# Kernel optimization log

Hardware: AMD Instinct MI355X
Metric: run time of the kernel (lower is better)

Reference implementation:

```python
import jax, jax.numpy as jnp
import numpy as np

BETA = 0.25  # commitment loss weight (standard VQ-VAE)


def setup_inputs() -> dict:
    key = jax.random.key(0)
    ks = jax.random.split(key, 6)
    B, C, H, W = 8, 64, 64, 64
    K = 8192  # codebook size
    return {
        "z": jax.random.normal(ks[0], (B, C, H, W), dtype=jnp.float32),
        "pre_w": jax.random.normal(ks[1], (C, C), dtype=jnp.float32) * (1.0 / np.sqrt(C)),
        "pre_b": jax.random.normal(ks[2], (C,), dtype=jnp.float32) * 0.02,
        "emb": jax.random.normal(ks[3], (K, C), dtype=jnp.float32),
        "post_w": jax.random.normal(ks[4], (C, C), dtype=jnp.float32) * (1.0 / np.sqrt(C)),
        "post_b": jax.random.normal(ks[5], (C,), dtype=jnp.float32) * 0.02,
    }


def reference(z, pre_w, pre_b, emb, post_w, post_b):
    B, C, H, W = z.shape
    # pre_quant_conv: 1x1 conv == channel-mixing matmul
    ze = jnp.einsum("bchw,oc->bohw", z, pre_w) + pre_b[None, :, None, None]
    # flatten to tokens [N, C]
    zf = ze.transpose(0, 2, 3, 1).reshape(-1, C)
    # squared L2 distances to codebook: ||z||^2 - 2 z.e + ||e||^2
    d = (jnp.sum(zf * zf, axis=1, keepdims=True)
         - 2.0 * (zf @ emb.T)
         + jnp.sum(emb * emb, axis=1)[None, :])  # [N, K]
    idx = jnp.argmin(d, axis=1)  # [N]
    q = emb[idx].reshape(B, H, W, C).transpose(0, 3, 1, 2)  # [B,C,H,W]
    # VQ losses
    codebook_loss = jnp.mean((jax.lax.stop_gradient(ze) - q) ** 2)
    commit_loss = BETA * jnp.mean((ze - jax.lax.stop_gradient(q)) ** 2)
    loss = codebook_loss + commit_loss
    # straight-through estimator
    quant = ze + jax.lax.stop_gradient(q - ze)
    # post_quant_conv: 1x1 conv
    out = jnp.einsum("bchw,oc->bohw", quant, post_w) + post_b[None, :, None, None]
    return out, loss
```

## Files before the change

### kernel.cpp

```cpp
#include <hip/hip_runtime.h>
#include <stdint.h>

#define HW 4096
#define NTOK 32768
#define KCB 8192
#define YSPLIT 8
#define KCOV (KCB / YSPLIT)
#define NCHUNK (KCOV / 64)
#define MARGIN 0.0119628906f

typedef __bf16 bf16x8 __attribute__((ext_vector_type(8)));
typedef float f32x16 __attribute__((ext_vector_type(16)));
typedef unsigned int uint;
typedef unsigned short u16;
typedef unsigned long long u64;

static __device__ inline u16 f2bf(float f) {
    uint u = __float_as_uint(f);
    return (u16)((u + 0x7FFFu + ((u >> 16) & 1u)) >> 16);
}
static __device__ inline float bf2f(u16 h) {
    return __uint_as_float(((uint)h) << 16);
}
static __device__ inline uint fsort(float f) {
    uint u = __float_as_uint(f);
    return u ^ ((uint)((int)u >> 31) | 0x80000000u);
}
static __device__ inline uint umin2(uint a, uint b) { return a < b ? a : b; }
static __device__ inline uint umax2(uint a, uint b) { return a > b ? a : b; }
static __device__ inline uint umed3(uint a, uint b, uint c) {
    return umax2(umin2(a, b), umin2(umax2(a, b), c));
}

__global__ __launch_bounds__(256) void prep_kernel(
    const float* __restrict__ z, const float* __restrict__ pre_w,
    const float* __restrict__ pre_b, const float* __restrict__ emb,
    u16* __restrict__ zq, u16* __restrict__ embq,
    float* __restrict__ ee, float* __restrict__ eebs,
    float* __restrict__ loss_out, int* __restrict__ flagcnt)
{
    __shared__ __attribute__((aligned(16))) float wt[64 * 64];
    __shared__ __attribute__((aligned(16))) float zt[64 * 64];
    __shared__ float bls[64];
    const int t  = threadIdx.x;
    const int bx = blockIdx.x;

    if (bx >= 512) {
        const int k   = (bx - 512) * 32 + (t >> 3);
        const int sub = t & 7;
        const float4* er = (const float4*)(emb + (size_t)k * 64 + sub * 8);
        float4 v0 = er[0], v1 = er[1];

        float s = v0.x*v0.x + v0.y*v0.y + v0.z*v0.z + v0.w*v0.w
                + v1.x*v1.x + v1.y*v1.y + v1.z*v1.z + v1.w*v1.w;
        s += __shfl_xor(s, 1, 64);
        s += __shfl_xor(s, 2, 64);
        s += __shfl_xor(s, 4, 64);
        if (sub == 0) { ee[k] = s; eebs[k] = 1024.f * (256.f + s); }

        float vals[8] = {-64.f*v0.x, -64.f*v0.y, -64.f*v0.z, -64.f*v0.w,
                         -64.f*v1.x, -64.f*v1.y, -64.f*v1.z, -64.f*v1.w};
        u16 hb[8], lb[8];
        #pragma unroll
        for (int c = 0; c < 8; ++c) {
            hb[c] = f2bf(vals[c]);
            lb[c] = f2bf(vals[c] - bf2f(hb[c]));
        }
        uint4 uh, ul;
        uh.x = (uint)hb[0] | ((uint)hb[1] << 16);
        uh.y = (uint)hb[2] | ((uint)hb[3] << 16);
        uh.z = (uint)hb[4] | ((uint)hb[5] << 16);
        uh.w = (uint)hb[6] | ((uint)hb[7] << 16);
        ul.x = (uint)lb[0] | ((uint)lb[1] << 16);
        ul.y = (uint)lb[2] | ((uint)lb[3] << 16);
        ul.z = (uint)lb[4] | ((uint)lb[5] << 16);
        ul.w = (uint)lb[6] | ((uint)lb[7] << 16);

        const int sw = k & 7;
        uint4* out = (uint4*)(embq + (size_t)k * 128);
        out[sub ^ sw]       = uh;
        out[(8 + sub) ^ sw] = ul;
        if (bx == 512 && t == 0) { loss_out[0] = 0.f; *flagcnt = 0; }
        return;
    }

    const int tok0 = bx * 64;
    const int b    = tok0 >> 12;
    const int hw0  = tok0 & 4095;

    for (int i = t; i < 64 * 64; i += 256) {
        int o = i >> 6, c = i & 63;
        wt[c * 64 + o] = pre_w[i];
    }
    if (t < 64) bls[t] = pre_b[t];
    {
        const int tl = t & 63;
        #pragma unroll
        for (int rr = 0; rr < 16; ++rr) {
            const int c = (t >> 6) + rr * 4;
            zt[c * 64 + tl] = z[(size_t)b * (64 * HW) + (size_t)c * HW + hw0 + tl];
        }
    }
    __syncthreads();

    const int tok = t >> 2;
    const int og  = t & 3;
    const int n   = tok0 + tok;

    float acc[16];
    #pragma unroll
    for (int j = 0; j < 16; ++j) acc[j] = 0.f;

    for (int c = 0; c < 64; ++c) {
        const float zv = zt[c * 64 + tok];
        #pragma unroll
        for (int g = 0; g < 4; ++g) {
            float4 w4 = *(const float4*)(wt + c * 64 + og * 16 + g * 4);
            acc[g*4+0] = fmaf(zv, w4.x, acc[g*4+0]);
            acc[g*4+1] = fmaf(zv, w4.y, acc[g*4+1]);
            acc[g*4+2] = fmaf(zv, w4.z, acc[g*4+2]);
            acc[g*4+3] = fmaf(zv, w4.w, acc[g*4+3]);
        }
    }
    #pragma unroll
    for (int j = 0; j < 16; ++j) acc[j] = 32.f * (acc[j] + bls[og * 16 + j]);

    uint uh[8], ul[8];
    #pragma unroll
    for (int j = 0; j < 8; ++j) {
        float v0 = acc[2*j], v1 = acc[2*j+1];
        u16 h0 = f2bf(v0), h1 = f2bf(v1);
        u16 l0 = f2bf(v0 - bf2f(h0)), l1 = f2bf(v1 - bf2f(h1));
        uh[j] = (uint)h0 | ((uint)h1 << 16);
        ul[j] = (uint)l0 | ((uint)l1 << 16);
    }
    uint4* zh = (uint4*)(zq + (size_t)n * 128 + og * 16);
    uint4* zl = (uint4*)(zq + (size_t)n * 128 + 64 + og * 16);
    zh[0] = *(uint4*)&uh[0]; zh[1] = *(uint4*)&uh[4];
    zl[0] = *(uint4*)&ul[0]; zl[1] = *(uint4*)&ul[4];
}

__global__ __launch_bounds__(256, 4) void dist_kernel(
    const u16* __restrict__ zq, const u16* __restrict__ embq,
    const float* __restrict__ eebs, uint* __restrict__ halfbb,
    uint* __restrict__ halfss)
{
    __shared__ __attribute__((aligned(16))) char smem[32768];
    __shared__ uint gbk[128];

    const int t    = threadIdx.x;
    const int w    = t >> 6;
    const int l    = t & 63;
    const int col  = l & 31;
    const int half = l >> 5;
    const int tok0 = blockIdx.x * 128;
    const int y    = blockIdx.y;
    const int kbase = y * KCOV;

    bf16x8 ah[4], al[4];
    {
        const u16* zrow = zq + (size_t)(tok0 + w * 32 + col) * 128;
        #pragma unroll
        for (int s = 0; s < 4; ++s) {
            ah[s] = *(const bf16x8*)(zrow + s*16 + half*8);
            al[s] = *(const bf16x8*)(zrow + 64 + s*16 + half*8);
        }
    }

    const int sw = col & 7;
    int boh[4][2], bol[4][2];
    #pragma unroll
    for (int s = 0; s < 4; ++s)
        #pragma unroll
        for (int ct = 0; ct < 2; ++ct) {
            const int nl = ct * 32 + col;
            boh[s][ct] = nl * 256 + (((s*2 + half) ^ sw) << 4);
            bol[s][ct] = nl * 256 + (((8 + s*2 + half) ^ sw) << 4);
        }

    uint bb[16], ss[16];
    #pragma unroll
    for (int r = 0; r < 16; ++r) { bb[r] = 0xFFFFFFFFu; ss[r] = 0xFFFFFFFFu; }

    float e0 = eebs[kbase + col];
    float e1 = eebs[kbase + 32 + col];

    {
        const char* g = (const char*)embq + (size_t)kbase * 256;
        #pragma unroll
        for (int i = 0; i < 4; ++i) {
            int off = i * 4096 + t * 16;
            __builtin_amdgcn_global_load_lds(
                (const __attribute__((address_space(1))) void*)(g + off),
                (__attribute__((address_space(3))) void*)(smem + off), 16, 0, 0);
        }
    }

    for (int kt = 0; kt < NCHUNK; ++kt) {
        __syncthreads();
        if (kt + 1 < NCHUNK) {
            const char* g = (const char*)embq + (size_t)kbase * 256 + (size_t)(kt + 1) * 16384;
            char* ld = smem + ((kt + 1) & 1) * 16384;
            #pragma unroll
            for (int i = 0; i < 4; ++i) {
                int off = i * 4096 + t * 16;
                __builtin_amdgcn_global_load_lds(
                    (const __attribute__((address_space(1))) void*)(g + off),
                    (__attribute__((address_space(3))) void*)(ld + off), 16, 0, 0);
            }
        }
        const char* buf = smem + (kt & 1) * 16384;

        float e0n = 0.f, e1n = 0.f;
        if (kt + 1 < NCHUNK) {
            e0n = eebs[kbase + (kt+1)*64 + col];
            e1n = eebs[kbase + (kt+1)*64 + 32 + col];
        }

        f32x16 a0, a1;
        #pragma unroll
        for (int r = 0; r < 16; ++r) { a0[r] = e0; a1[r] = e1; }

        #pragma unroll
        for (int s = 0; s < 4; ++s) {
            bf16x8 bh0 = *(const bf16x8*)(buf + boh[s][0]);
            bf16x8 bh1 = *(const bf16x8*)(buf + boh[s][1]);
            bf16x8 bl0 = *(const bf16x8*)(buf + bol[s][0]);
            bf16x8 bl1 = *(const bf16x8*)(buf + bol[s][1]);
            a0 = __builtin_amdgcn_mfma_f32_32x32x16_bf16(ah[s], bh0, a0, 0, 0, 0);
            a1 = __builtin_amdgcn_mfma_f32_32x32x16_bf16(ah[s], bh1, a1, 0, 0, 0);
            a0 = __builtin_amdgcn_mfma_f32_32x32x16_bf16(ah[s], bl0, a0, 0, 0, 0);
            a1 = __builtin_amdgcn_mfma_f32_32x32x16_bf16(ah[s], bl1, a1, 0, 0, 0);
            a0 = __builtin_amdgcn_mfma_f32_32x32x16_bf16(al[s], bh0, a0, 0, 0, 0);
            a1 = __builtin_amdgcn_mfma_f32_32x32x16_bf16(al[s], bh1, a1, 0, 0, 0);
        }

        const uint i0 = (uint)(kt * 64 + col);
        const uint i1 = i0 + 32;
        #pragma unroll
        for (int r = 0; r < 16; ++r) {
            const uint p0 = (((uint)a0[r]) << 10) + i0;
            const uint p1 = (((uint)a1[r]) << 10) + i1;
            ss[r] = umin2(ss[r], umed3(bb[r], p0, p1));
            bb[r] = umin2(umin2(bb[r], p0), p1);
        }
        e0 = e0n; e1 = e1n;
    }

    __syncthreads();
    uint* keyt = (uint*)smem;
    #pragma unroll
    for (int r = 0; r < 16; ++r) {
        const int tl = w*32 + (r & 3) + 8*(r >> 2) + 4*half;
        keyt[tl * 32 + col] = bb[r];
    }
    __syncthreads();
    if (t < 128) {
        uint gb = keyt[t * 32 + (t & 31)];
        #pragma unroll 4
        for (int j = 1; j < 32; ++j)
            gb = umin2(gb, keyt[t * 32 + ((j + t) & 31)]);
        gbk[t] = gb;
    }
    __syncthreads();
    #pragma unroll
    for (int r = 0; r < 16; ++r) {
        const int tl = w*32 + (r & 3) + 8*(r >> 2) + 4*half;
        const uint mykey = bb[r];
        keyt[tl * 32 + col] = (mykey == gbk[tl]) ? ss[r] : mykey;
    }
    __syncthreads();
    if (t < 128) {
        uint sv = keyt[t * 32 + (t & 31)];
        #pragma unroll 4
        for (int j = 1; j < 32; ++j)
            sv = umin2(sv, keyt[t * 32 + ((j + t) & 31)]);
        halfbb[(size_t)y * NTOK + tok0 + t] = gbk[t];
        halfss[(size_t)y * NTOK + tok0 + t] = sv;
    }
}

__global__ __launch_bounds__(256) void merge_kernel(
    const uint* __restrict__ halfbb, const uint* __restrict__ halfss,
    uint* __restrict__ bestidx, u64* __restrict__ bestkeyB,
    int* __restrict__ flagcnt, int* __restrict__ flaglist)
{
    const int n = blockIdx.x * 256 + threadIdx.x;
    uint m1 = 0xFFFFFFFFu, m2 = 0xFFFFFFFFu, smin = 0xFFFFFFFFu;
    int ywin = 0;
    #pragma unroll
    for (int y = 0; y < YSPLIT; ++y) {
        const uint kb = halfbb[(size_t)y * NTOK + n];
        if (kb < m1) { m2 = m1; m1 = kb; ywin = y; }
        else if (kb < m2) m2 = kb;
        smin = umin2(smin, halfss[(size_t)y * NTOK + n]);
    }
    const uint bv_u = m1 >> 10;
    const uint sv_u = umin2(m2, smin) >> 10;
    const float gap = (float)(sv_u - bv_u) * 9.765625e-4f;
    const bool flag = (gap < MARGIN) | (bv_u < (128u << 10));
    bestidx[n]  = flag ? 0xFFFFFFFFu : (uint)(ywin * 1024) + (m1 & 1023u);
    bestkeyB[n] = ~0ull;
    if (flag) {
        int pos = atomicAdd(flagcnt, 1);
        flaglist[pos] = n;
    }
}

__global__ __launch_bounds__(256) void cleanup_kernel(
    const u16* __restrict__ zq, const float* __restrict__ emb,
    const float* __restrict__ ee, const int* __restrict__ flagcnt,
    const int* __restrict__ flaglist, u64* __restrict__ bestkeyB)
{
    __shared__ __attribute__((aligned(16))) float zf[64];
    __shared__ u64 smin;
    const int cnt = *flagcnt;
    const int t = threadIdx.x;

    for (int job = blockIdx.x; job < cnt * 32; job += 2048) {
        const int fi    = job >> 5;
        const int slice = job & 31;
        const int tok   = flaglist[fi];
        if (t == 0) smin = ~0ull;
        if (t < 64) {
            const u16* zr = zq + (size_t)tok * 128;
            zf[t] = (bf2f(zr[t]) + bf2f(zr[64 + t])) * 0.03125f;
        }
        __syncthreads();

        const int k = slice * 256 + t;
        const float4* er = (const float4*)(emb + (size_t)k * 64);
        float d = 0.f;
        #pragma unroll
        for (int jj = 0; jj < 16; ++jj) {
            float4 e = er[jj];
            float4 zv = *(const float4*)&zf[4*jj];
            d = fmaf(e.x, zv.x, fmaf(e.y, zv.y, fmaf(e.z, zv.z, fmaf(e.w, zv.w, d))));
        }
        float dd = fmaf(-2.f, d, ee[k]);
        u64 key = ((u64)fsort(dd) << 32) | (uint)k;
        #pragma unroll
        for (int off = 32; off > 0; off >>= 1) {
            u64 o = __shfl_down(key, off, 64);
            key = (o < key) ? o : key;
        }
        if ((t & 63) == 0) atomicMin(&smin, key);
        __syncthreads();
        if (t == 0) atomicMin(&bestkeyB[tok], smin);
        __syncthreads();
    }
}

__global__ __launch_bounds__(256) void gather_kernel(
    const float* __restrict__ emb, const uint* __restrict__ bestidx,
    const u64* __restrict__ bestkeyB, const u16* __restrict__ zq,
    const float* __restrict__ post_w, const float* __restrict__ post_b,
    float* __restrict__ out, float* __restrict__ loss_out)
{
    __shared__ __attribute__((aligned(16))) float wt[64 * 64];
    __shared__ __attribute__((aligned(16))) float qt[64 * 64];
    __shared__ float bls[64];
    __shared__ int idxs[64];
    __shared__ float red[4];
    const int t = threadIdx.x;
    const int tok0 = blockIdx.x * 64;
    const int b    = tok0 >> 12;
    const int hw0  = tok0 & 4095;

    if (t < 64) {
        const uint raw = bestidx[tok0 + t];
        idxs[t] = (raw == 0xFFFFFFFFu) ? (int)(bestkeyB[tok0 + t] & 0xFFFFFFFFull)
                                       : (int)raw;
        bls[t] = post_b[t];
    }
    for (int i = t; i < 64 * 64; i += 256) {
        int o = i >> 6, c = i & 63;
        wt[c * 64 + o] = post_w[i];
    }
    __syncthreads();

    const int tok = t >> 2;
    const int og  = t & 3;
    const int n   = tok0 + tok;

    {
        const float4* qr = (const float4*)(emb + (size_t)idxs[tok] * 64);
        #pragma unroll
        for (int p = 0; p < 4; ++p) {
            const int c0 = og * 16 + p * 4;
            float4 v = qr[c0 >> 2];
            qt[(c0+0) * 64 + tok] = v.x;
            qt[(c0+1) * 64 + tok] = v.y;
            qt[(c0+2) * 64 + tok] = v.z;
            qt[(c0+3) * 64 + tok] = v.w;
        }
    }
    __syncthreads();

    float lsum = 0.f;
    {
        const uint4* zh = (const uint4*)(zq + (size_t)n * 128 + og * 16);
        const uint4* zl = (const uint4*)(zq + (size_t)n * 128 + 64 + og * 16);
        #pragma unroll
        for (int h = 0; h < 2; ++h) {
            uint4 uh = zh[h], ul = zl[h];
            const uint uhv[4] = {uh.x, uh.y, uh.z, uh.w};
            const uint ulv[4] = {ul.x, ul.y, ul.z, ul.w};
            #pragma unroll
            for (int p = 0; p < 4; ++p) {
                const int c = og * 16 + h * 8 + p * 2;
                float z0 = (bf2f((u16)(uhv[p] & 0xFFFF)) + bf2f((u16)(ulv[p] & 0xFFFF))) * 0.03125f;
                float z1 = (bf2f((u16)(uhv[p] >> 16))    + bf2f((u16)(ulv[p] >> 16)))    * 0.03125f;
                float d0 = z0 - qt[c * 64 + tok];
                float d1 = z1 - qt[(c + 1) * 64 + tok];
                lsum += d0 * d0 + d1 * d1;
            }
        }
    }

    {
        const int w    = t >> 6;
        const int lane = t & 63;
        float acc[16];
        #pragma unroll
        for (int j = 0; j < 16; ++j) acc[j] = 0.f;

        for (int c = 0; c < 64; ++c) {
            const float qv = qt[c * 64 + lane];
            #pragma unroll
            for (int g = 0; g < 4; ++g) {
                float4 w4 = *(const float4*)(wt + c * 64 + w * 16 + g * 4);
                acc[g*4+0] = fmaf(qv, w4.x, acc[g*4+0]);
                acc[g*4+1] = fmaf(qv, w4.y, acc[g*4+1]);
                acc[g*4+2] = fmaf(qv, w4.z, acc[g*4+2]);
                acc[g*4+3] = fmaf(qv, w4.w, acc[g*4+3]);
            }
        }
        float* op = out + (size_t)b * (64 * HW) + hw0 + lane;
        #pragma unroll
        for (int j = 0; j < 16; ++j)
            op[(size_t)(w * 16 + j) * HW] = acc[j] + bls[w * 16 + j];
    }

    #pragma unroll
    for (int off = 32; off > 0; off >>= 1) lsum += __shfl_down(lsum, off, 64);
    if ((t & 63) == 0) red[t >> 6] = lsum;
    __syncthreads();
    if (t == 0) {
        const float tot = red[0] + red[1] + red[2] + red[3];
        atomicAdd(loss_out, tot * (1.25f / 2097152.f));
    }
}

extern "C" void kernel_launch(void* const* d_in, const int* in_sizes, int n_in,
                              void* d_out, int out_size, void* d_ws, size_t ws_size,
                              hipStream_t stream)
{
    const float* z      = (const float*)d_in[0];
    const float* pre_w  = (const float*)d_in[1];
    const float* pre_b  = (const float*)d_in[2];
    const float* emb    = (const float*)d_in[3];
    const float* post_w = (const float*)d_in[4];
    const float* post_b = (const float*)d_in[5];
    float* outp = (float*)d_out;
    float* loss_out = outp + (size_t)NTOK * 64;

    u16*   zq       = (u16*)d_ws;
    float* ee       = (float*)(zq + (size_t)NTOK * 128);
    float* eebs     = ee + KCB;
    u16*   embq     = (u16*)(eebs + KCB);
    u64*   bestkeyB = (u64*)(embq + (size_t)KCB * 128);
    uint*  bestidx  = (uint*)(bestkeyB + NTOK);
    int*   flagcnt  = (int*)(bestidx + NTOK);
    int*   flaglist = flagcnt + 1;
    uint*  halfbb   = (uint*)(flaglist + NTOK);
    uint*  halfss   = halfbb + (size_t)YSPLIT * NTOK;

    prep_kernel<<<768, 256, 0, stream>>>(z, pre_w, pre_b, emb, zq, embq, ee, eebs,
                                         loss_out, flagcnt);
    dist_kernel<<<dim3(NTOK / 128, YSPLIT), 256, 0, stream>>>(zq, embq, eebs, halfbb, halfss);
    merge_kernel<<<NTOK / 256, 256, 0, stream>>>(halfbb, halfss, bestidx, bestkeyB,
                                                 flagcnt, flaglist);
    cleanup_kernel<<<2048, 256, 0, stream>>>(zq, emb, ee, flagcnt, flaglist, bestkeyB);
    gather_kernel<<<NTOK / 64, 256, 0, stream>>>(emb, bestidx, bestkeyB, zq,
                                                 post_w, post_b, outp, loss_out);
}
```

Baseline: 234.0 us.

## Fuse merge, cleanup and gather into one persistent kernel with grid barriers

Replaces the merge, cleanup and gather kernels with a single finish kernel of 512 blocks. The blocks coordinate through two software grid barriers built on atomics in workspace memory, which prep_kernel resets. This removes two kernel launches and the bestidx round trip through global memory, since the per-token index stays in shared memory. In exchange, the barriers need all 512 blocks to be resident at the same time (launch_bounds 256,2), and cleanup now runs on 512 blocks instead of 2048, so the flagged-token recompute has less parallelism.

```diff
diff --git a/kernel.cpp b/kernel.cpp
--- a/kernel.cpp
+++ b/kernel.cpp
@@ -7,6 +7,7 @@
 #define YSPLIT 8
 #define KCOV (KCB / YSPLIT)
 #define NCHUNK (KCOV / 64)
+#define FIN_BLOCKS 512
 #define MARGIN 0.0119628906f
 
 typedef __bf16 bf16x8 __attribute__((ext_vector_type(8)));
@@ -32,12 +33,28 @@
     return umax2(umin2(a, b), umin2(umax2(a, b), c));
 }
 
+static __device__ inline void grid_barrier(int* cnt, int* rel) {
+    __syncthreads();
+    if (threadIdx.x == 0) {
+        __threadfence();
+        int old = atomicAdd(cnt, 1);
+        if (old == FIN_BLOCKS - 1) {
+            atomicExch(rel, 1);
+        } else {
+            while (atomicAdd(rel, 0) == 0) __builtin_amdgcn_s_sleep(8);
+        }
+        __threadfence();
+    }
+    __syncthreads();
+}
+
 __global__ __launch_bounds__(256) void prep_kernel(
     const float* __restrict__ z, const float* __restrict__ pre_w,
     const float* __restrict__ pre_b, const float* __restrict__ emb,
     u16* __restrict__ zq, u16* __restrict__ embq,
     float* __restrict__ ee, float* __restrict__ eebs,
-    float* __restrict__ loss_out, int* __restrict__ flagcnt)
+    float* __restrict__ loss_out, int* __restrict__ flagcnt,
+    int* __restrict__ barw)
 {
     __shared__ __attribute__((aligned(16))) float wt[64 * 64];
     __shared__ __attribute__((aligned(16))) float zt[64 * 64];
@@ -80,7 +97,12 @@
         uint4* out = (uint4*)(embq + (size_t)k * 128);
         out[sub ^ sw]       = uh;
         out[(8 + sub) ^ sw] = ul;
-        if (bx == 512 && t == 0) { loss_out[0] = 0.f; *flagcnt = 0; }
+        if (bx == 512 && t == 0) {
+            loss_out[0] = 0.f;
+            atomicExch(flagcnt, 0);
+            atomicExch(&barw[0], 0); atomicExch(&barw[1], 0);
+            atomicExch(&barw[2], 0); atomicExch(&barw[3], 0);
+        }
         return;
     }
 
@@ -280,103 +302,99 @@
     }
 }
 
-__global__ __launch_bounds__(256) void merge_kernel(
+__global__ __launch_bounds__(256, 2) void finish_kernel(
+    const float* __restrict__ emb, const float* __restrict__ ee,
     const uint* __restrict__ halfbb, const uint* __restrict__ halfss,
-    uint* __restrict__ bestidx, u64* __restrict__ bestkeyB,
-    int* __restrict__ flagcnt, int* __restrict__ flaglist)
-{
-    const int n = blockIdx.x * 256 + threadIdx.x;
-    uint m1 = 0xFFFFFFFFu, m2 = 0xFFFFFFFFu, smin = 0xFFFFFFFFu;
-    int ywin = 0;
-    #pragma unroll
-    for (int y = 0; y < YSPLIT; ++y) {
-        const uint kb = halfbb[(size_t)y * NTOK + n];
-        if (kb < m1) { m2 = m1; m1 = kb; ywin = y; }
-        else if (kb < m2) m2 = kb;
-        smin = umin2(smin, halfss[(size_t)y * NTOK + n]);
-    }
-    const uint bv_u = m1 >> 10;
-    const uint sv_u = umin2(m2, smin) >> 10;
-    const float gap = (float)(sv_u - bv_u) * 9.765625e-4f;
-    const bool flag = (gap < MARGIN) | (bv_u < (128u << 10));
-    bestidx[n]  = flag ? 0xFFFFFFFFu : (uint)(ywin * 1024) + (m1 & 1023u);
-    bestkeyB[n] = ~0ull;
-    if (flag) {
-        int pos = atomicAdd(flagcnt, 1);
-        flaglist[pos] = n;
-    }
-}
-
-__global__ __launch_bounds__(256) void cleanup_kernel(
-    const u16* __restrict__ zq, const float* __restrict__ emb,
-    const float* __restrict__ ee, const int* __restrict__ flagcnt,
-    const int* __restrict__ flaglist, u64* __restrict__ bestkeyB)
-{
-    __shared__ __attribute__((aligned(16))) float zf[64];
-    __shared__ u64 smin;
-    const int cnt = *flagcnt;
-    const int t = threadIdx.x;
-
-    for (int job = blockIdx.x; job < cnt * 32; job += 2048) {
-        const int fi    = job >> 5;
-        const int slice = job & 31;
-        const int tok   = flaglist[fi];
-        if (t == 0) smin = ~0ull;
-        if (t < 64) {
-            const u16* zr = zq + (size_t)tok * 128;
-            zf[t] = (bf2f(zr[t]) + bf2f(zr[64 + t])) * 0.03125f;
-        }
-        __syncthreads();
-
-        const int k = slice * 256 + t;
-        const float4* er = (const float4*)(emb + (size_t)k * 64);
-        float d = 0.f;
-        #pragma unroll
-        for (int jj = 0; jj < 16; ++jj) {
-            float4 e = er[jj];
-            float4 zv = *(const float4*)&zf[4*jj];
-            d = fmaf(e.x, zv.x, fmaf(e.y, zv.y, fmaf(e.z, zv.z, fmaf(e.w, zv.w, d))));
-        }
-        float dd = fmaf(-2.f, d, ee[k]);
-        u64 key = ((u64)fsort(dd) << 32) | (uint)k;
-        #pragma unroll
-        for (int off = 32; off > 0; off >>= 1) {
-            u64 o = __shfl_down(key, off, 64);
-            key = (o < key) ? o : key;
-        }
-        if ((t & 63) == 0) atomicMin(&smin, key);
-        __syncthreads();
-        if (t == 0) atomicMin(&bestkeyB[tok], smin);
-        __syncthreads();
-    }
-}
-
-__global__ __launch_bounds__(256) void gather_kernel(
-    const float* __restrict__ emb, const uint* __restrict__ bestidx,
-    const u64* __restrict__ bestkeyB, const u16* __restrict__ zq,
-    const float* __restrict__ post_w, const float* __restrict__ post_b,
-    float* __restrict__ out, float* __restrict__ loss_out)
+    const u16* __restrict__ zq, const float* __restrict__ post_w,
+    const float* __restrict__ post_b, float* __restrict__ out,
+    float* __restrict__ loss_out, u64* __restrict__ bestkeyB,
+    int* __restrict__ flagcnt, int* __restrict__ flaglist,
+    int* __restrict__ barw)
 {
     __shared__ __attribute__((aligned(16))) float wt[64 * 64];
     __shared__ __attribute__((aligned(16))) float qt[64 * 64];
     __shared__ float bls[64];
     __shared__ int idxs[64];
     __shared__ float red[4];
+    __shared__ u64 skey;
     const int t = threadIdx.x;
     const int tok0 = blockIdx.x * 64;
     const int b    = tok0 >> 12;
     const int hw0  = tok0 & 4095;
-
-    if (t < 64) {
-        const uint raw = bestidx[tok0 + t];
-        idxs[t] = (raw == 0xFFFFFFFFu) ? (int)(bestkeyB[tok0 + t] & 0xFFFFFFFFull)
-                                       : (int)raw;
-        bls[t] = post_b[t];
-    }
+    float* zf = qt;
+
     for (int i = t; i < 64 * 64; i += 256) {
         int o = i >> 6, c = i & 63;
         wt[c * 64 + o] = post_w[i];
     }
+    if (t < 64) {
+        bls[t] = post_b[t];
+        const int n = tok0 + t;
+        uint m1 = 0xFFFFFFFFu, m2 = 0xFFFFFFFFu, smin = 0xFFFFFFFFu;
+        int ywin = 0;
+        #pragma unroll
+        for (int y = 0; y < YSPLIT; ++y) {
+            const uint kb = halfbb[(size_t)y * NTOK + n];
+            if (kb < m1) { m2 = m1; m1 = kb; ywin = y; }
+            else if (kb < m2) m2 = kb;
+            smin = umin2(smin, halfss[(size_t)y * NTOK + n]);
+        }
+        const uint bv_u = m1 >> 10;
+        const uint sv_u = umin2(m2, smin) >> 10;
+        const float gap = (float)(sv_u - bv_u) * 9.765625e-4f;
+        const bool flag = (gap < MARGIN) | (bv_u < (128u << 10));
+        if (flag) {
+            idxs[t] = -1;
+            atomicExch(&bestkeyB[n], ~0ull);
+            int pos = atomicAdd(flagcnt, 1);
+            atomicExch(&flaglist[pos], n);
+        } else {
+            idxs[t] = (int)((uint)(ywin * 1024) + (m1 & 1023u));
+        }
+    }
+
+    grid_barrier(&barw[0], &barw[1]);
+
+    {
+        const int fcnt = atomicAdd(flagcnt, 0);
+        for (int job = blockIdx.x; job < fcnt * 32; job += FIN_BLOCKS) {
+            const int fi    = job >> 5;
+            const int slice = job & 31;
+            const int tok   = atomicAdd(&flaglist[fi], 0);
+            if (t == 0) skey = ~0ull;
+            if (t < 64) {
+                const u16* zr = zq + (size_t)tok * 128;
+                zf[t] = (bf2f(zr[t]) + bf2f(zr[64 + t])) * 0.03125f;
+            }
+            __syncthreads();
+
+            const int k = slice * 256 + t;
+            const float4* er = (const float4*)(emb + (size_t)k * 64);
+            float d = 0.f;
+            #pragma unroll
+            for (int jj = 0; jj < 16; ++jj) {
+                float4 e = er[jj];
+                float4 zv = *(const float4*)&zf[4*jj];
+                d = fmaf(e.x, zv.x, fmaf(e.y, zv.y, fmaf(e.z, zv.z, fmaf(e.w, zv.w, d))));
+            }
+            float dd = fmaf(-2.f, d, ee[k]);
+            u64 key = ((u64)fsort(dd) << 32) | (uint)k;
+            #pragma unroll
+            for (int off = 32; off > 0; off >>= 1) {
+                u64 o = __shfl_down(key, off, 64);
+                key = (o < key) ? o : key;
+            }
+            if ((t & 63) == 0) atomicMin(&skey, key);
+            __syncthreads();
+            if (t == 0) atomicMin(&bestkeyB[tok], skey);
+            __syncthreads();
+        }
+    }
+
+    grid_barrier(&barw[2], &barw[3]);
+
+    if (t < 64 && idxs[t] < 0)
+        idxs[t] = (int)(atomicAdd(&bestkeyB[tok0 + t], 0ull) & 0xFFFFFFFFull);
     __syncthreads();
 
     const int tok = t >> 2;
@@ -470,18 +488,16 @@
     float* eebs     = ee + KCB;
     u16*   embq     = (u16*)(eebs + KCB);
     u64*   bestkeyB = (u64*)(embq + (size_t)KCB * 128);
-    uint*  bestidx  = (uint*)(bestkeyB + NTOK);
-    int*   flagcnt  = (int*)(bestidx + NTOK);
-    int*   flaglist = flagcnt + 1;
+    int*   flagcnt  = (int*)(bestkeyB + NTOK);
+    int*   barw     = flagcnt + 1;
+    int*   flaglist = barw + 4;
     uint*  halfbb   = (uint*)(flaglist + NTOK);
     uint*  halfss   = halfbb + (size_t)YSPLIT * NTOK;
 
     prep_kernel<<<768, 256, 0, stream>>>(z, pre_w, pre_b, emb, zq, embq, ee, eebs,
-                                         loss_out, flagcnt);
+                                         loss_out, flagcnt, barw);
     dist_kernel<<<dim3(NTOK / 128, YSPLIT), 256, 0, stream>>>(zq, embq, eebs, halfbb, halfss);
-    merge_kernel<<<NTOK / 256, 256, 0, stream>>>(halfbb, halfss, bestidx, bestkeyB,
-                                                 flagcnt, flaglist);
-    cleanup_kernel<<<2048, 256, 0, stream>>>(zq, emb, ee, flagcnt, flaglist, bestkeyB);
-    gather_kernel<<<NTOK / 64, 256, 0, stream>>>(emb, bestidx, bestkeyB, zq,
-                                                 post_w, post_b, outp, loss_out);
-}
+    finish_kernel<<<FIN_BLOCKS, 256, 0, stream>>>(emb, ee, halfbb, halfss, zq,
+                                                  post_w, post_b, outp, loss_out,
+                                                  bestkeyB, flagcnt, flaglist, barw);
+}
```

Result: slower. 314.2 us (+34.3%).

## Precompute post-conv over codebook and gather projected rows in finish kernel

Applied to the files above, without the earlier changes.

Since the output is post_w applied to a codebook row plus bias, the change applies the post 1x1 conv to all 8192 codebook entries once, in extra prep_kernel blocks. The final kernel then only gathers the precomputed rows for each token instead of running a per-token 64x64 matmul. This replaces work over 32768 tokens with work over 8192 codes and drops the weight staging in the last kernel. It costs an extra 2MB workspace buffer, 128 more prep blocks, and a second gather of raw emb rows for the loss.

```diff
diff --git a/kernel.cpp b/kernel.cpp
--- a/kernel.cpp
+++ b/kernel.cpp
@@ -35,15 +35,78 @@
 __global__ __launch_bounds__(256) void prep_kernel(
     const float* __restrict__ z, const float* __restrict__ pre_w,
     const float* __restrict__ pre_b, const float* __restrict__ emb,
+    const float* __restrict__ post_w, const float* __restrict__ post_b,
     u16* __restrict__ zq, u16* __restrict__ embq,
     float* __restrict__ ee, float* __restrict__ eebs,
-    float* __restrict__ loss_out, int* __restrict__ flagcnt)
+    float* __restrict__ embWb, float* __restrict__ loss_out,
+    int* __restrict__ flagcnt)
 {
     __shared__ __attribute__((aligned(16))) float wt[64 * 64];
     __shared__ __attribute__((aligned(16))) float zt[64 * 64];
     __shared__ float bls[64];
     const int t  = threadIdx.x;
     const int bx = blockIdx.x;
+
+    if (bx >= 768) {
+        const int k0  = (bx - 768) * 64;
+        const int tok = t >> 2;
+        const int og  = t & 3;
+
+        for (int i = t; i < 64 * 64; i += 256) {
+            int o = i >> 6, c = i & 63;
+            wt[c * 64 + o] = post_w[i];
+        }
+        if (t < 64) bls[t] = post_b[t];
+        {
+            const float4* qr = (const float4*)(emb + (size_t)(k0 + tok) * 64);
+            #pragma unroll
+            for (int p = 0; p < 4; ++p) {
+                const int c0 = og * 16 + p * 4;
+                float4 v = qr[c0 >> 2];
+                zt[(c0+0) * 64 + tok] = v.x;
+                zt[(c0+1) * 64 + tok] = v.y;
+                zt[(c0+2) * 64 + tok] = v.z;
+                zt[(c0+3) * 64 + tok] = v.w;
+            }
+        }
+        __syncthreads();
+
+        const int w    = t >> 6;
+        const int lane = t & 63;
+        float acc[16];
+        #pragma unroll
+        for (int j = 0; j < 16; ++j) acc[j] = 0.f;
+        for (int c = 0; c < 64; ++c) {
+            const float qv = zt[c * 64 + lane];
+            #pragma unroll
+            for (int g = 0; g < 4; ++g) {
+                float4 w4 = *(const float4*)(wt + c * 64 + w * 16 + g * 4);
+                acc[g*4+0] = fmaf(qv, w4.x, acc[g*4+0]);
+                acc[g*4+1] = fmaf(qv, w4.y, acc[g*4+1]);
+                acc[g*4+2] = fmaf(qv, w4.z, acc[g*4+2]);
+                acc[g*4+3] = fmaf(qv, w4.w, acc[g*4+3]);
+            }
+        }
+        __syncthreads();
+        #pragma unroll
+        for (int j = 0; j < 16; ++j)
+            zt[(w * 16 + j) * 64 + lane] = acc[j] + bls[w * 16 + j];
+        __syncthreads();
+        {
+            float4* orow = (float4*)(embWb + (size_t)(k0 + tok) * 64 + og * 16);
+            #pragma unroll
+            for (int p = 0; p < 4; ++p) {
+                const int c0 = og * 16 + p * 4;
+                float4 v;
+                v.x = zt[(c0+0) * 64 + tok];
+                v.y = zt[(c0+1) * 64 + tok];
+                v.z = zt[(c0+2) * 64 + tok];
+                v.w = zt[(c0+3) * 64 + tok];
+                orow[p] = v;
+            }
+        }
+        return;
+    }
 
     if (bx >= 512) {
         const int k   = (bx - 512) * 32 + (t >> 3);
@@ -351,15 +414,13 @@
     }
 }
 
-__global__ __launch_bounds__(256) void gather_kernel(
-    const float* __restrict__ emb, const uint* __restrict__ bestidx,
-    const u64* __restrict__ bestkeyB, const u16* __restrict__ zq,
-    const float* __restrict__ post_w, const float* __restrict__ post_b,
-    float* __restrict__ out, float* __restrict__ loss_out)
+__global__ __launch_bounds__(256) void finish_kernel(
+    const float* __restrict__ emb, const float* __restrict__ embWb,
+    const uint* __restrict__ bestidx, const u64* __restrict__ bestkeyB,
+    const u16* __restrict__ zq, float* __restrict__ out,
+    float* __restrict__ loss_out)
 {
-    __shared__ __attribute__((aligned(16))) float wt[64 * 64];
-    __shared__ __attribute__((aligned(16))) float qt[64 * 64];
-    __shared__ float bls[64];
+    __shared__ __attribute__((aligned(16))) float ot[64 * 64];
     __shared__ int idxs[64];
     __shared__ float red[4];
     const int t = threadIdx.x;
@@ -371,75 +432,58 @@
         const uint raw = bestidx[tok0 + t];
         idxs[t] = (raw == 0xFFFFFFFFu) ? (int)(bestkeyB[tok0 + t] & 0xFFFFFFFFull)
                                        : (int)raw;
-        bls[t] = post_b[t];
-    }
-    for (int i = t; i < 64 * 64; i += 256) {
-        int o = i >> 6, c = i & 63;
-        wt[c * 64 + o] = post_w[i];
     }
     __syncthreads();
 
     const int tok = t >> 2;
     const int og  = t & 3;
     const int n   = tok0 + tok;
+    const int idx = idxs[tok];
 
     {
-        const float4* qr = (const float4*)(emb + (size_t)idxs[tok] * 64);
+        const float4* orow = (const float4*)(embWb + (size_t)idx * 64 + og * 16);
         #pragma unroll
         for (int p = 0; p < 4; ++p) {
             const int c0 = og * 16 + p * 4;
-            float4 v = qr[c0 >> 2];
-            qt[(c0+0) * 64 + tok] = v.x;
-            qt[(c0+1) * 64 + tok] = v.y;
-            qt[(c0+2) * 64 + tok] = v.z;
-            qt[(c0+3) * 64 + tok] = v.w;
-        }
-    }
-    __syncthreads();
+            float4 v = orow[p];
+            ot[(c0+0) * 64 + tok] = v.x;
+            ot[(c0+1) * 64 + tok] = v.y;
+            ot[(c0+2) * 64 + tok] = v.z;
+            ot[(c0+3) * 64 + tok] = v.w;
+        }
+    }
 
     float lsum = 0.f;
     {
+        const float4* qr = (const float4*)(emb + (size_t)idx * 64 + og * 16);
         const uint4* zh = (const uint4*)(zq + (size_t)n * 128 + og * 16);
         const uint4* zl = (const uint4*)(zq + (size_t)n * 128 + 64 + og * 16);
         #pragma unroll
         for (int h = 0; h < 2; ++h) {
             uint4 uh = zh[h], ul = zl[h];
+            float4 q0 = qr[h*2], q1 = qr[h*2+1];
             const uint uhv[4] = {uh.x, uh.y, uh.z, uh.w};
             const uint ulv[4] = {ul.x, ul.y, ul.z, ul.w};
+            const float qv[8] = {q0.x, q0.y, q0.z, q0.w, q1.x, q1.y, q1.z, q1.w};
             #pragma unroll
             for (int p = 0; p < 4; ++p) {
-                const int c = og * 16 + h * 8 + p * 2;
                 float z0 = (bf2f((u16)(uhv[p] & 0xFFFF)) + bf2f((u16)(ulv[p] & 0xFFFF))) * 0.03125f;
                 float z1 = (bf2f((u16)(uhv[p] >> 16))    + bf2f((u16)(ulv[p] >> 16)))    * 0.03125f;
-                float d0 = z0 - qt[c * 64 + tok];
-                float d1 = z1 - qt[(c + 1) * 64 + tok];
+                float d0 = z0 - qv[2*p];
+                float d1 = z1 - qv[2*p+1];
                 lsum += d0 * d0 + d1 * d1;
             }
         }
     }
+    __syncthreads();
 
     {
         const int w    = t >> 6;
         const int lane = t & 63;
-        float acc[16];
-        #pragma unroll
-        for (int j = 0; j < 16; ++j) acc[j] = 0.f;
-
-        for (int c = 0; c < 64; ++c) {
-            const float qv = qt[c * 64 + lane];
-            #pragma unroll
-            for (int g = 0; g < 4; ++g) {
-                float4 w4 = *(const float4*)(wt + c * 64 + w * 16 + g * 4);
-                acc[g*4+0] = fmaf(qv, w4.x, acc[g*4+0]);
-                acc[g*4+1] = fmaf(qv, w4.y, acc[g*4+1]);
-                acc[g*4+2] = fmaf(qv, w4.z, acc[g*4+2]);
-                acc[g*4+3] = fmaf(qv, w4.w, acc[g*4+3]);
-            }
-        }
         float* op = out + (size_t)b * (64 * HW) + hw0 + lane;
         #pragma unroll
         for (int j = 0; j < 16; ++j)
-            op[(size_t)(w * 16 + j) * HW] = acc[j] + bls[w * 16 + j];
+            op[(size_t)(w * 16 + j) * HW] = ot[(w * 16 + j) * 64 + lane];
     }
 
     #pragma unroll
@@ -475,13 +519,14 @@
     int*   flaglist = flagcnt + 1;
     uint*  halfbb   = (uint*)(flaglist + NTOK);
     uint*  halfss   = halfbb + (size_t)YSPLIT * NTOK;
-
-    prep_kernel<<<768, 256, 0, stream>>>(z, pre_w, pre_b, emb, zq, embq, ee, eebs,
-                                         loss_out, flagcnt);
+    float* embWb    = (float*)(halfss + (size_t)YSPLIT * NTOK);
+
+    prep_kernel<<<896, 256, 0, stream>>>(z, pre_w, pre_b, emb, post_w, post_b,
+                                         zq, embq, ee, eebs, embWb, loss_out, flagcnt);
     dist_kernel<<<dim3(NTOK / 128, YSPLIT), 256, 0, stream>>>(zq, embq, eebs, halfbb, halfss);
     merge_kernel<<<NTOK / 256, 256, 0, stream>>>(halfbb, halfss, bestidx, bestkeyB,
                                                  flagcnt, flaglist);
     cleanup_kernel<<<2048, 256, 0, stream>>>(zq, emb, ee, flagcnt, flaglist, bestkeyB);
-    gather_kernel<<<NTOK / 64, 256, 0, stream>>>(emb, bestidx, bestkeyB, zq,
-                                                 post_w, post_b, outp, loss_out);
-}
+    finish_kernel<<<NTOK / 64, 256, 0, stream>>>(emb, embWb, bestidx, bestkeyB, zq,
+                                                 outp, loss_out);
+}
```

After: 230.2 us. No clear change (-1.6%).
